# Kernel tuning notes

Measured on AMD Instinct MI355X. Metric: run time of the kernel, lower is better.

The kernel has to match this reference:

```python
import jax, jax.numpy as jnp
import numpy as np

def _dct_mat():
    k = np.arange(8)[:, None]
    n = np.arange(8)[None, :]
    norm = np.where(k == 0, np.sqrt(1.0 / 8.0), np.sqrt(2.0 / 8.0))
    return jnp.asarray(norm * np.cos(np.pi / 8.0 * (n + 0.5) * k), jnp.float32)

_LUM = np.array([[16,11,10,16,24,40,51,61],[12,12,14,19,26,58,60,55],[14,13,16,24,40,57,69,56],[14,17,22,29,51,87,80,62],[18,22,37,56,68,109,103,77],[24,35,55,64,81,104,113,92],[49,64,78,87,103,121,120,101],[72,92,95,98,112,100,103,99]], np.float32)
_CHROM = np.array([[17,18,24,47,99,99,99,99],[18,21,26,66,99,99,99,99],[24,26,56,99,99,99,99,99],[47,66,99,99,99,99,99,99],[99,99,99,99,99,99,99,99],[99,99,99,99,99,99,99,99],[99,99,99,99,99,99,99,99],[99,99,99,99,99,99,99,99]], np.float32)

def _qtables(quality):
    q = max(1, min(100, int(quality)))
    scale = 5000.0 / q if q < 50 else 200.0 - 2.0 * q
    tbs = np.stack([_LUM, _CHROM]) * scale
    tbs = np.clip((tbs + 50.0) / 100.0, 1.0, 255.0)
    return jnp.asarray(tbs, jnp.float32)

def _jpeg_forward(img, quality):
    bs, _, oh, ow = img.shape
    x = img * 255.0
    pad_h = (8 - oh % 8) % 8
    pad_w = (8 - ow % 8) % 8
    if pad_h or pad_w:
        x = jnp.pad(x, ((0, 0), (0, 0), (0, pad_h), (0, pad_w)), mode='edge')
    h, w = oh + pad_h, ow + pad_w
    W_ycc = jnp.asarray([[0.299, 0.587, 0.114], [-0.1687, -0.3313, 0.5], [0.5, -0.4187, -0.0813]], jnp.float32)
    b_ycc = jnp.asarray([0.0, 128.0, 128.0], jnp.float32)
    # 1x1 conv colorspace transform
    yuv = jnp.einsum('oc,bchw->bohw', W_ycc, x) + b_ycc[None, :, None, None]
    nb = bs * 3
    hb, wb = h // 8, w // 8
    # unfold(kernel=8, stride=8) == non-overlapping 8x8 blocking, block-row-major
    blocks = yuv.reshape(nb, hb, 8, wb, 8).transpose(0, 1, 3, 2, 4).reshape(nb, hb * wb, 8, 8)
    M = _dct_mat()
    dct = jnp.matmul(M, jnp.matmul(blocks - 128.0, M.T))
    qt = _qtables(quality)
    # faithful to original slicing patches_dct[:bs] / [bs:] over the flattened (b,c) dim
    row = jnp.arange(nb)[:, None, None, None]
    qfull = jnp.where(row < bs, qt[0], qt[1])
    t = dct / qfull
    # straight-through round
    tq = (t + jax.lax.stop_gradient(jnp.round(t) - t)) * qfull
    idct = jnp.matmul(M.T, jnp.matmul(tq, M)) + 128.0
    rec = idct.reshape(nb, hb, wb, 8, 8).transpose(0, 1, 3, 2, 4).reshape(bs, 3, h, w)
    rec = rec - b_ycc[None, :, None, None]
    y, cb, cr = rec[:, 0], rec[:, 1], rec[:, 2]
    r = y + 1.402 * cr
    g = y - 0.34414 * cb - 0.71414 * cr
    b = y + 1.772 * cb
    rgb = jnp.stack([r, g, b], axis=1)[:, :, :oh, :ow]
    return jnp.clip(rgb / 255.0, 0.0, 1.0)

def setup_inputs() -> dict:
    key = jax.random.key(0)
    img = jax.random.uniform(key, (16, 3, 512, 512), dtype=jnp.float32)
    return {"img": img, "quality": 80}

def reference(img, quality):
    return _jpeg_forward(img, quality)
```

## Files before the change

kernel.cpp:

```cpp
#include <hip/hip_runtime.h>
#include <math.h>

#define C1 0.9807852804032304
#define C2 0.9238795325112867
#define C3 0.8314696123025452
#define C4 0.7071067811865476
#define C5 0.5555702330196022
#define C6 0.3826834323650898
#define C7 0.19509032201612825
#define N0 0.35355339059327373

static constexpr double Mc[8][8] = {
 {  N0,      N0,      N0,      N0,      N0,      N0,      N0,      N0    },
 {  .5*C1,   .5*C3,   .5*C5,   .5*C7,  -.5*C7,  -.5*C5,  -.5*C3,  -.5*C1 },
 {  .5*C2,   .5*C6,  -.5*C6,  -.5*C2,  -.5*C2,  -.5*C6,   .5*C6,   .5*C2 },
 {  .5*C3,  -.5*C7,  -.5*C1,  -.5*C5,   .5*C5,   .5*C1,   .5*C7,  -.5*C3 },
 {  .5*C4,  -.5*C4,  -.5*C4,   .5*C4,   .5*C4,  -.5*C4,  -.5*C4,   .5*C4 },
 {  .5*C5,  -.5*C1,   .5*C7,   .5*C3,  -.5*C3,  -.5*C7,   .5*C1,  -.5*C5 },
 {  .5*C6,  -.5*C2,   .5*C2,  -.5*C6,  -.5*C6,   .5*C2,  -.5*C2,   .5*C6 },
 {  .5*C7,  -.5*C5,   .5*C3,  -.5*C1,   .5*C1,  -.5*C3,   .5*C5,  -.5*C7 },
};
#define ROWF(r) {(float)Mc[r][0],(float)Mc[r][1],(float)Mc[r][2],(float)Mc[r][3],\
                 (float)Mc[r][4],(float)Mc[r][5],(float)Mc[r][6],(float)Mc[r][7]}
static constexpr float Mcf[8][8] = {ROWF(0),ROWF(1),ROWF(2),ROWF(3),ROWF(4),ROWF(5),ROWF(6),ROWF(7)};

static __device__ const double LUM_BASE[64] = {
 16,11,10,16,24,40,51,61,
 12,12,14,19,26,58,60,55,
 14,13,16,24,40,57,69,56,
 14,17,22,29,51,87,80,62,
 18,22,37,56,68,109,103,77,
 24,35,55,64,81,104,113,92,
 49,64,78,87,103,121,120,101,
 72,92,95,98,112,100,103,99};
static __device__ const double CHROM_BASE[64] = {
 17,18,24,47,99,99,99,99,
 18,21,26,66,99,99,99,99,
 24,26,56,99,99,99,99,99,
 47,66,99,99,99,99,99,99,
 99,99,99,99,99,99,99,99,
 99,99,99,99,99,99,99,99,
 99,99,99,99,99,99,99,99,
 99,99,99,99,99,99,99,99};

#define WAVE_FENCE() asm volatile("s_waitcnt lgkmcnt(0)" ::: "memory")

__global__ __launch_bounds__(64, 5) void jpeg_fwd(const float* __restrict__ img,
                                                  const int* __restrict__ quality,
                                                  float* __restrict__ out)
{
    __shared__ double QR[256];
    union UBuf {
        double d64[576];
        float  f32[576];
    };
    __shared__ UBuf UB;

    const int l   = threadIdx.x;
    const int blk = l >> 3;
    const int rr  = l & 7;

    const int b    = blockIdx.x >> 9;
    const int rem  = blockIdx.x & 511;
    const int row0 = (rem >> 3) << 3;
    const int col0 = (rem & 7) << 6;

    const size_t plane = 512 * 512;

    const float* p = img + (size_t)(b * 3) * plane + (size_t)(row0 + rr) * 512 + col0 + blk * 8;
    float4 R0 = *(const float4*)(p);
    float4 R1 = *(const float4*)(p + 4);
    float4 G0 = *(const float4*)(p + plane);
    float4 G1 = *(const float4*)(p + plane + 4);
    float4 B0 = *(const float4*)(p + 2 * plane);
    float4 B1 = *(const float4*)(p + 2 * plane + 4);

    {
        int q = quality[0];
        q = q < 1 ? 1 : (q > 100 ? 100 : q);
        double scale = (q < 50) ? (5000.0 / (double)q) : (200.0 - 2.0 * (double)q);
        #pragma unroll
        for (int h = 0; h < 2; ++h) {
            int e = l + (h << 6);
            int tbl = e >> 6, idx = e & 63;
            double base = tbl ? CHROM_BASE[idx] : LUM_BASE[idx];
            double v = (base * scale + 50.0) / 100.0;
            v = fmin(fmax(v, 1.0), 255.0);
            QR[2 * e]     = v;
            QR[2 * e + 1] = 1.0 / v;
        }
    }
    WAVE_FENCE();

    const double F00 =  0.299 * 255.0,  F01 =  0.587 * 255.0,  F02 =  0.114 * 255.0;
    const double F10 = -0.1687 * 255.0, F11 = -0.3313 * 255.0, F12 =  0.5 * 255.0;
    const double F20 =  0.5 * 255.0,    F21 = -0.4187 * 255.0, F22 = -0.0813 * 255.0;

    float rf[8] = {R0.x, R0.y, R0.z, R0.w, R1.x, R1.y, R1.z, R1.w};
    float gf[8] = {G0.x, G0.y, G0.z, G0.w, G1.x, G1.y, G1.z, G1.w};
    float bf[8] = {B0.x, B0.y, B0.z, B0.w, B1.x, B1.y, B1.z, B1.w};

    float pix0[8], pix1[8], pix2[8];

#define CHANNEL_BODY(CIDX, PIXARR, COLOR_EXPR)                                  \
    {                                                                           \
           \
        const int sel_c = ((b * 3 + CIDX) < 16) ? 0 : 1;                        \
        const double* QRb = QR + (((sel_c << 6) + rr) << 1);                    \
           \
        double row[8];                                                          \
        _Pragma("unroll")                                                       \
        for (int k = 0; k < 8; ++k) {                                           \
            double rv = (double)rf[k];                                          \
            double gv = (double)gf[k];                                          \
            double bv = (double)bf[k];                                          \
            double v  = (COLOR_EXPR);                                           \
            row[k] = v - 128.0;                                                 \
        }                                                                       \
                            \
        double y[8];                                                            \
        {                                                                       \
            double u0[4], v0[4];                                                \
            _Pragma("unroll")                                                   \
            for (int k = 0; k < 4; ++k) {                                       \
                u0[k] = row[k] + row[7 - k];                                    \
                v0[k] = row[k] - row[7 - k];                                    \
            }                                                                   \
            _Pragma("unroll")                                                   \
            for (int c = 0; c < 8; c += 2) {                                    \
                double se = 0.0, so = 0.0;                                      \
                _Pragma("unroll")                                               \
                for (int k = 0; k < 4; ++k) {                                   \
                    se += u0[k] * Mc[c][k];                                     \
                    so += v0[k] * Mc[c + 1][k];                                 \
                }                                                               \
                y[c] = se; y[c + 1] = so;                                       \
            }                                                                   \
        }                                                                       \
                            \
        {                                                                       \
            double* tb = UB.d64 + blk * 72 + rr * 9;                            \
            _Pragma("unroll")                                                   \
            for (int k = 0; k < 8; ++k) tb[k] = y[k];                           \
        }                                                                       \
        WAVE_FENCE();                                                           \
        double t1[8];                                                           \
        {                                                                       \
            const double* tb = UB.d64 + blk * 72 + rr;                          \
            _Pragma("unroll")                                                   \
            for (int k = 0; k < 8; ++k) t1[k] = tb[k * 9];                      \
        }                                                                       \
        WAVE_FENCE(); \
         \
         \
         \
        double wq[8];                                                           \
        {                                                                       \
            double tu[4], tv[4];                                                \
            _Pragma("unroll")                                                   \
            for (int k = 0; k < 4; ++k) {                                       \
                tu[k] = t1[k] + t1[7 - k];                                      \
                tv[k] = t1[k] - t1[7 - k];                                      \
            }                                                                   \
            _Pragma("unroll")                                                   \
            for (int j = 0; j < 8; j += 2) {                                    \
                double se = 0.0, so = 0.0;                                      \
                _Pragma("unroll")                                               \
                for (int k = 0; k < 4; ++k) {                                   \
                    se += tu[k] * Mc[j][k];                                     \
                    so += tv[k] * Mc[j + 1][k];                                 \
                }                                                               \
                {     \
                    double q = QRb[(j << 4)];                                   \
                    double r = QRb[(j << 4) + 1];                               \
                    double qh = se * r;                                         \
                    double e  = fma(-q, qh, se);                                \
                    double qq = fma(e, r, qh);                                  \
                    wq[j] = rint(qq) * q;                                       \
                }                                                               \
                {                                                    \
                    double q = QRb[((j + 1) << 4)];                             \
                    double r = QRb[((j + 1) << 4) + 1];                         \
                    double qh = so * r;                                         \
                    double e  = fma(-q, qh, so);                                \
                    double qq = fma(e, r, qh);                                  \
                    wq[j + 1] = rint(qq) * q;                                   \
                }                                                               \
            }                                                                   \
        }                                                                       \
                                         \
        float wqf[8];                                                           \
        _Pragma("unroll")                                                       \
        for (int k = 0; k < 8; ++k) wqf[k] = (float)wq[k];                      \
               \
        float a3[8];                                                            \
        _Pragma("unroll")                                                       \
        for (int j = 0; j < 4; ++j) {                                           \
            float pe = 0.0f, po = 0.0f;                                         \
            _Pragma("unroll")                                                   \
            for (int k = 0; k < 4; ++k) {                                       \
                pe += wqf[2 * k]     * Mcf[2 * k][j];                           \
                po += wqf[2 * k + 1] * Mcf[2 * k + 1][j];                       \
            }                                                                   \
            a3[j]     = pe + po;                                                \
            a3[7 - j] = pe - po;                                                \
        }                                                                       \
           \
        {                                                                       \
            float* tb = UB.f32 + blk * 72 + rr * 9;                             \
            _Pragma("unroll")                                                   \
            for (int k = 0; k < 8; ++k) tb[k] = a3[k];                          \
        }                                                                       \
        WAVE_FENCE();                                                           \
        float tC[8];                                                            \
        {                                                                       \
            const float* c2 = UB.f32 + blk * 72 + rr;                           \
            _Pragma("unroll")                                                   \
            for (int k = 0; k < 8; ++k) tC[k] = c2[k * 9];                      \
        }                                                                       \
               \
        _Pragma("unroll")                                                       \
        for (int j = 0; j < 4; ++j) {                                           \
            float e = 0.0f, o = 0.0f;                                           \
            _Pragma("unroll")                                                   \
            for (int k = 0; k < 4; ++k) {                                       \
                e += tC[2 * k]     * Mcf[2 * k][j];                             \
                o += tC[2 * k + 1] * Mcf[2 * k + 1][j];                         \
            }                                                                   \
            PIXARR[j]     = e + o;                                              \
            PIXARR[7 - j] = e - o;                                              \
        }                                                                       \
        WAVE_FENCE(); \
    }

    CHANNEL_BODY(0, pix0, F00 * rv + F01 * gv + F02 * bv)
    CHANNEL_BODY(1, pix1, F10 * rv + F11 * gv + F12 * bv + 128.0)
    CHANNEL_BODY(2, pix2, F20 * rv + F21 * gv + F22 * bv + 128.0)
#undef CHANNEL_BODY

    float oR[8], oG[8], oB[8];
    #pragma unroll
    for (int k = 0; k < 8; ++k) {
        float yd = pix0[k] + 128.0f;
        float vR = yd + 1.402f * pix2[k];
        float vG = yd - 0.34414f * pix1[k] - 0.71414f * pix2[k];
        float vB = yd + 1.772f * pix1[k];
        oR[k] = fminf(fmaxf(vR * (1.0f / 255.0f), 0.0f), 1.0f);
        oG[k] = fminf(fmaxf(vG * (1.0f / 255.0f), 0.0f), 1.0f);
        oB[k] = fminf(fmaxf(vB * (1.0f / 255.0f), 0.0f), 1.0f);
    }

    const size_t rowoff = (size_t)(row0 + rr) * 512 + col0 + blk * 8;
    float* qR = out + (size_t)(b * 3 + 0) * plane + rowoff;
    float* qG = out + (size_t)(b * 3 + 1) * plane + rowoff;
    float* qB = out + (size_t)(b * 3 + 2) * plane + rowoff;
    *(float4*)(qR)     = make_float4(oR[0], oR[1], oR[2], oR[3]);
    *(float4*)(qR + 4) = make_float4(oR[4], oR[5], oR[6], oR[7]);
    *(float4*)(qG)     = make_float4(oG[0], oG[1], oG[2], oG[3]);
    *(float4*)(qG + 4) = make_float4(oG[4], oG[5], oG[6], oG[7]);
    *(float4*)(qB)     = make_float4(oB[0], oB[1], oB[2], oB[3]);
    *(float4*)(qB + 4) = make_float4(oB[4], oB[5], oB[6], oB[7]);
}

extern "C" void kernel_launch(void* const* d_in, const int* in_sizes, int n_in,
                              void* d_out, int out_size, void* d_ws, size_t ws_size,
                              hipStream_t stream) {
    const float* img     = (const float*)d_in[0];
    const int*   quality = (const int*)d_in[1];
    float*       out     = (float*)d_out;
    jpeg_fwd<<<8192, 64, 0, stream>>>(img, quality, out);
}
```

Measured before the change: 105.8 us.

## Process two strips per block with software-prefetched loads of the next strip

Each 64-thread block now handles two consecutive 8x64 strips in a loop, launching half as many blocks. The global loads for the second strip are issued after the first channel's DCT work, so memory latency overlaps with computation, and the q-table setup is amortized over two strips. Launch bounds drop from 5 to 4 waves per SIMD to allow the extra live registers, at the cost of lower occupancy.

```diff
diff --git a/kernel.cpp b/kernel.cpp
--- a/kernel.cpp
+++ b/kernel.cpp
@@ -45,7 +45,7 @@
 
 #define WAVE_FENCE() asm volatile("s_waitcnt lgkmcnt(0)" ::: "memory")
 
-__global__ __launch_bounds__(64, 5) void jpeg_fwd(const float* __restrict__ img,
+__global__ __launch_bounds__(64, 4) void jpeg_fwd(const float* __restrict__ img,
                                                   const int* __restrict__ quality,
                                                   float* __restrict__ out)
 {
@@ -60,20 +60,19 @@
     const int blk = l >> 3;
     const int rr  = l & 7;
 
-    const int b    = blockIdx.x >> 9;
-    const int rem  = blockIdx.x & 511;
-    const int row0 = (rem >> 3) << 3;
-    const int col0 = (rem & 7) << 6;
-
     const size_t plane = 512 * 512;
 
-    const float* p = img + (size_t)(b * 3) * plane + (size_t)(row0 + rr) * 512 + col0 + blk * 8;
-    float4 R0 = *(const float4*)(p);
-    float4 R1 = *(const float4*)(p + 4);
-    float4 G0 = *(const float4*)(p + plane);
-    float4 G1 = *(const float4*)(p + plane + 4);
-    float4 B0 = *(const float4*)(p + 2 * plane);
-    float4 B1 = *(const float4*)(p + 2 * plane + 4);
+    int sid = blockIdx.x << 1;
+
+    const float* p0 = img + (size_t)((sid >> 9) * 3) * plane
+                    + (size_t)((((sid & 511) >> 3) << 3) + rr) * 512
+                    + ((sid & 7) << 6) + blk * 8;
+    float4 Rc0 = *(const float4*)(p0);
+    float4 Rc1 = *(const float4*)(p0 + 4);
+    float4 Gc0 = *(const float4*)(p0 + plane);
+    float4 Gc1 = *(const float4*)(p0 + plane + 4);
+    float4 Bc0 = *(const float4*)(p0 + 2 * plane);
+    float4 Bc1 = *(const float4*)(p0 + 2 * plane + 4);
 
     {
         int q = quality[0];
@@ -95,12 +94,6 @@
     const double F00 =  0.299 * 255.0,  F01 =  0.587 * 255.0,  F02 =  0.114 * 255.0;
     const double F10 = -0.1687 * 255.0, F11 = -0.3313 * 255.0, F12 =  0.5 * 255.0;
     const double F20 =  0.5 * 255.0,    F21 = -0.4187 * 255.0, F22 = -0.0813 * 255.0;
-
-    float rf[8] = {R0.x, R0.y, R0.z, R0.w, R1.x, R1.y, R1.z, R1.w};
-    float gf[8] = {G0.x, G0.y, G0.z, G0.w, G1.x, G1.y, G1.z, G1.w};
-    float bf[8] = {B0.x, B0.y, B0.z, B0.w, B1.x, B1.y, B1.z, B1.w};
-
-    float pix0[8], pix1[8], pix2[8];
 
 #define CHANNEL_BODY(CIDX, PIXARR, COLOR_EXPR)                                  \
     {                                                                           \
@@ -230,36 +223,71 @@
             PIXARR[j]     = e + o;                                              \
             PIXARR[7 - j] = e - o;                                              \
         }                                                                       \
-        WAVE_FENCE(); \
+        WAVE_FENCE();        \
     }
 
-    CHANNEL_BODY(0, pix0, F00 * rv + F01 * gv + F02 * bv)
-    CHANNEL_BODY(1, pix1, F10 * rv + F11 * gv + F12 * bv + 128.0)
-    CHANNEL_BODY(2, pix2, F20 * rv + F21 * gv + F22 * bv + 128.0)
+    #pragma unroll 1
+    for (int s = 0; s < 2; ++s, ++sid) {
+        const int b    = sid >> 9;
+        const int rem  = sid & 511;
+        const int row0 = (rem >> 3) << 3;
+        const int col0 = (rem & 7) << 6;
+
+        float rf[8] = {Rc0.x, Rc0.y, Rc0.z, Rc0.w, Rc1.x, Rc1.y, Rc1.z, Rc1.w};
+        float gf[8] = {Gc0.x, Gc0.y, Gc0.z, Gc0.w, Gc1.x, Gc1.y, Gc1.z, Gc1.w};
+        float bf[8] = {Bc0.x, Bc0.y, Bc0.z, Bc0.w, Bc1.x, Bc1.y, Bc1.z, Bc1.w};
+
+        float pix0[8], pix1[8], pix2[8];
+        float4 Rn0, Rn1, Gn0, Gn1, Bn0, Bn1;
+
+        CHANNEL_BODY(0, pix0, F00 * rv + F01 * gv + F02 * bv)
+
+        if (s == 0) {
+            const int sn = sid + 1;
+            const float* pn = img + (size_t)((sn >> 9) * 3) * plane
+                            + (size_t)((((sn & 511) >> 3) << 3) + rr) * 512
+                            + ((sn & 7) << 6) + blk * 8;
+            Rn0 = *(const float4*)(pn);
+            Rn1 = *(const float4*)(pn + 4);
+            Gn0 = *(const float4*)(pn + plane);
+            Gn1 = *(const float4*)(pn + plane + 4);
+            Bn0 = *(const float4*)(pn + 2 * plane);
+            Bn1 = *(const float4*)(pn + 2 * plane + 4);
+        }
+
+        CHANNEL_BODY(1, pix1, F10 * rv + F11 * gv + F12 * bv + 128.0)
+        CHANNEL_BODY(2, pix2, F20 * rv + F21 * gv + F22 * bv + 128.0)
+
+        float oR[8], oG[8], oB[8];
+        #pragma unroll
+        for (int k = 0; k < 8; ++k) {
+            float yd = pix0[k] + 128.0f;
+            float vR = yd + 1.402f * pix2[k];
+            float vG = yd - 0.34414f * pix1[k] - 0.71414f * pix2[k];
+            float vB = yd + 1.772f * pix1[k];
+            oR[k] = fminf(fmaxf(vR * (1.0f / 255.0f), 0.0f), 1.0f);
+            oG[k] = fminf(fmaxf(vG * (1.0f / 255.0f), 0.0f), 1.0f);
+            oB[k] = fminf(fmaxf(vB * (1.0f / 255.0f), 0.0f), 1.0f);
+        }
+
+        const size_t rowoff = (size_t)(row0 + rr) * 512 + col0 + blk * 8;
+        float* qR = out + (size_t)(b * 3 + 0) * plane + rowoff;
+        float* qG = out + (size_t)(b * 3 + 1) * plane + rowoff;
+        float* qB = out + (size_t)(b * 3 + 2) * plane + rowoff;
+        *(float4*)(qR)     = make_float4(oR[0], oR[1], oR[2], oR[3]);
+        *(float4*)(qR + 4) = make_float4(oR[4], oR[5], oR[6], oR[7]);
+        *(float4*)(qG)     = make_float4(oG[0], oG[1], oG[2], oG[3]);
+        *(float4*)(qG + 4) = make_float4(oG[4], oG[5], oG[6], oG[7]);
+        *(float4*)(qB)     = make_float4(oB[0], oB[1], oB[2], oB[3]);
+        *(float4*)(qB + 4) = make_float4(oB[4], oB[5], oB[6], oB[7]);
+
+        if (s == 0) {
+            Rc0 = Rn0; Rc1 = Rn1;
+            Gc0 = Gn0; Gc1 = Gn1;
+            Bc0 = Bn0; Bc1 = Bn1;
+        }
+    }
 #undef CHANNEL_BODY
-
-    float oR[8], oG[8], oB[8];
-    #pragma unroll
-    for (int k = 0; k < 8; ++k) {
-        float yd = pix0[k] + 128.0f;
-        float vR = yd + 1.402f * pix2[k];
-        float vG = yd - 0.34414f * pix1[k] - 0.71414f * pix2[k];
-        float vB = yd + 1.772f * pix1[k];
-        oR[k] = fminf(fmaxf(vR * (1.0f / 255.0f), 0.0f), 1.0f);
-        oG[k] = fminf(fmaxf(vG * (1.0f / 255.0f), 0.0f), 1.0f);
-        oB[k] = fminf(fmaxf(vB * (1.0f / 255.0f), 0.0f), 1.0f);
-    }
-
-    const size_t rowoff = (size_t)(row0 + rr) * 512 + col0 + blk * 8;
-    float* qR = out + (size_t)(b * 3 + 0) * plane + rowoff;
-    float* qG = out + (size_t)(b * 3 + 1) * plane + rowoff;
-    float* qB = out + (size_t)(b * 3 + 2) * plane + rowoff;
-    *(float4*)(qR)     = make_float4(oR[0], oR[1], oR[2], oR[3]);
-    *(float4*)(qR + 4) = make_float4(oR[4], oR[5], oR[6], oR[7]);
-    *(float4*)(qG)     = make_float4(oG[0], oG[1], oG[2], oG[3]);
-    *(float4*)(qG + 4) = make_float4(oG[4], oG[5], oG[6], oG[7]);
-    *(float4*)(qB)     = make_float4(oB[0], oB[1], oB[2], oB[3]);
-    *(float4*)(qB + 4) = make_float4(oB[4], oB[5], oB[6], oB[7]);
 }
 
 extern "C" void kernel_launch(void* const* d_in, const int* in_sizes, int n_in,
@@ -268,5 +296,5 @@
     const float* img     = (const float*)d_in[0];
     const int*   quality = (const int*)d_in[1];
     float*       out     = (float*)d_out;
-    jpeg_fwd<<<8192, 64, 0, stream>>>(img, quality, out);
+    jpeg_fwd<<<4096, 64, 0, stream>>>(img, quality, out);
 }
```

After: 104.5 us, median of 2. No clear change (-1.2%).
